# Kernel tuning notes

Hardware: AMD Instinct MI355X
Metric: run time of the kernel (lower is better)

Reference implementation:

```python
import jax, jax.numpy as jnp
import numpy as np

B, N, LATENT, HIDDEN = 65536, 32, 32, 64

def setup_inputs() -> dict:
    key = jax.random.key(0)
    ks = jax.random.split(key, 16)
    def xavier(k, shape):
        fan_in, fan_out = shape[1], shape[0]
        lim = float(np.sqrt(6.0 / (fan_in + fan_out)))
        return jax.random.uniform(k, shape, jnp.float32, -lim, lim)
    inp = {
        'x_sensors': jax.random.normal(ks[0], (B, N), jnp.float32),
        'state_x': jax.random.uniform(ks[1], (B, 1), jnp.float32),
        # GAT: W Linear(1, LATENT, bias=False), a Linear(2*LATENT, 1, bias=False), xavier init
        'W_gat': xavier(ks[2], (LATENT, 1)),
        'a_gat': xavier(ks[3], (1, 2 * LATENT)),
        # pooling: Linear(LATENT, LATENT//2) -> Tanh -> Linear(LATENT//2, 1) -> Softmax(dim=1)
        'p1_w': xavier(ks[4], (LATENT // 2, LATENT)),
        'p1_b': jnp.zeros((LATENT // 2,), jnp.float32),
        'p2_w': xavier(ks[5], (1, LATENT // 2)),
        'p2_b': jnp.zeros((1,), jnp.float32),
        # MNN: MonotonicLinear raw weights uniform(-0.5, 0.5), zero bias
        'm1_w': jax.random.uniform(ks[6], (HIDDEN, 1), jnp.float32, -0.5, 0.5),
        'm1_b': jnp.zeros((HIDDEN,), jnp.float32),
        'm2_w': jax.random.uniform(ks[7], (HIDDEN, HIDDEN), jnp.float32, -0.5, 0.5),
        'm2_b': jnp.zeros((HIDDEN,), jnp.float32),
        'm3_w': jax.random.uniform(ks[8], (LATENT, HIDDEN), jnp.float32, -0.5, 0.5),
        'm3_b': jnp.zeros((LATENT,), jnp.float32),
    }
    return inp

def reference(x_sensors, state_x, W_gat, a_gat, p1_w, p1_b, p2_w, p2_b,
              m1_w, m1_b, m2_w, m2_b, m3_w, m3_b):
    # --- GAT encoder ---
    # h = x_sensors[..., None] (B,N,1); Wh = h @ W_gat.T -> (B,N,D)
    Wh = jnp.einsum('bn,d->bnd', x_sensors, W_gat[:, 0])
    # e_ij = leakyrelu(a^T [Wh_i || Wh_j]) decomposed: a = [a1; a2]
    a1, a2 = a_gat[0, :LATENT], a_gat[0, LATENT:]
    s_i = jnp.einsum('bnd,d->bn', Wh, a1)  # contribution of Wh_i
    s_j = jnp.einsum('bnd,d->bn', Wh, a2)  # contribution of Wh_j
    e = jax.nn.leaky_relu(s_i[:, :, None] + s_j[:, None, :], 0.2)  # (B,N,N)
    alpha = jax.nn.softmax(e, axis=2)  # dropout is identity in eval
    h_prime = jnp.einsum('bij,bjd->bid', alpha, Wh)  # (B,N,D)
    # pooling: softmax over sensor dim (dim=1)
    t = jnp.tanh(h_prime @ p1_w.T + p1_b)
    beta = jax.nn.softmax(t @ p2_w.T + p2_b, axis=1)  # (B,N,1)
    z_enc = jnp.sum(h_prime * beta, axis=1)  # (B,D)
    # --- MNN decoder (exp-positive weights) ---
    h1 = jnp.tanh(state_x @ jnp.exp(m1_w).T + m1_b)
    h2 = jnp.tanh(h1 @ jnp.exp(m2_w).T + m2_b)
    z_dec = h2 @ jnp.exp(m3_w).T + m3_b  # (B,D)
    return (z_enc, z_dec)
```

## Files before the change

### kernel.cpp

```cpp
#include <hip/hip_runtime.h>
#include <hip/hip_bf16.h>

#define LOG2E     1.4426950408889634f
#define TWO_LOG2E 2.8853900817779268f

typedef __attribute__((ext_vector_type(8))) short    bf16x8;
typedef __attribute__((ext_vector_type(8))) _Float16 f16x8;
typedef __attribute__((ext_vector_type(4))) float    f32x4;
typedef __attribute__((ext_vector_type(2))) float    f32x2;

__device__ __forceinline__ float rcp_(float x){ return __builtin_amdgcn_rcpf(x); }
__device__ __forceinline__ float ex2_(float x){ return __builtin_amdgcn_exp2f(x); }

template<int K>
__device__ __forceinline__ float quadbc(float v){
  constexpr int ctrl = K * 0x55;
  return __int_as_float(__builtin_amdgcn_mov_dpp(__float_as_int(v), ctrl, 0xf, 0xf, true));
}

union FragB { bf16x8 v; uint32_t w[4]; uint4 u4; };
union FragH { f16x8  v; uint32_t w[4]; uint4 u4; };

__device__ __forceinline__ uint16_t f2bf(float x){
  union { __hip_bfloat16 h; uint16_t u; } c; c.h = __float2bfloat16(x); return c.u;
}
__device__ __forceinline__ float bf2f(uint16_t u){
  union { __hip_bfloat16 h; uint16_t u; } c; c.u = u; return __bfloat162float(c.h);
}
__device__ __forceinline__ uint32_t pkh(float a, float b){
  union { _Float16 h; uint16_t u; } ca, cb;
  ca.h = (_Float16)a; cb.h = (_Float16)b;
  return (uint32_t)ca.u | ((uint32_t)cb.u << 16);
}
__device__ __forceinline__ void split2(float a, float b, uint32_t& whi, uint32_t& wlo){
  uint16_t ah = f2bf(a), bh = f2bf(b);
  uint16_t al = f2bf(a - bf2f(ah)), bl_ = f2bf(b - bf2f(bh));
  whi = (uint32_t)ah | ((uint32_t)bh << 16);
  wlo = (uint32_t)al | ((uint32_t)bl_ << 16);
}
__device__ __forceinline__ void expsplit8(const float* __restrict__ src,
                                          FragB& hi, FragB& lo){
  float4 a = *(const float4*)src;
  float4 b = *(const float4*)(src + 4);
  float e0=__expf(a.x), e1=__expf(a.y), e2=__expf(a.z), e3=__expf(a.w);
  float e4=__expf(b.x), e5=__expf(b.y), e6=__expf(b.z), e7=__expf(b.w);
  split2(e0,e1, hi.w[0], lo.w[0]);
  split2(e2,e3, hi.w[1], lo.w[1]);
  split2(e4,e5, hi.w[2], lo.w[2]);
  split2(e6,e7, hi.w[3], lo.w[3]);
}
__device__ __forceinline__ void exph8(const float* __restrict__ src, FragH& out){
  float4 a = *(const float4*)src;
  float4 b = *(const float4*)(src + 4);
  out.w[0] = pkh(__expf(a.x), __expf(a.y));
  out.w[1] = pkh(__expf(a.z), __expf(a.w));
  out.w[2] = pkh(__expf(b.x), __expf(b.y));
  out.w[3] = pkh(__expf(b.z), __expf(b.w));
}

#define WS_FG1   0
#define WS_FG2H  2048
#define WS_FG2L  3072
#define WS_TBL   4096
#define WS_E1S   4608
#define WS_M1B   4672
#define WS_SCAL  4736

#define TBL_N     512
#define TBL_SCALE 25.6f
#define TBL_LO    -10.0f
#define TBL_CMAX  9.9f

__global__ __launch_bounds__(256) void IDSSM_pre(
    const float* __restrict__ Wg,  const float* __restrict__ ag,
    const float* __restrict__ p1w, const float* __restrict__ p1b,
    const float* __restrict__ p2w, const float* __restrict__ p2b,
    const float* __restrict__ m1w, const float* __restrict__ m1b,
    const float* __restrict__ m2w, const float* __restrict__ m3w,
    float* __restrict__ ws)
{
  const int blk = blockIdx.x;
  const int tid = threadIdx.x;
  const int l  = tid & 63;
  const int bl = l & 15, gt = l >> 4;
  if (blk < 2){
    const int s  = (blk*256 + tid) >> 6;
    const int mt = s >> 1, kt = s & 1;
    FragH h;
    exph8(m2w + (bl + 16*mt)*64 + 8*gt + 32*kt, h);
    *(uint4*)(ws + WS_FG1 + (size_t)(s*64 + l)*4) = h.u4;
  } else if (blk == 2){
    const int s2  = tid >> 6;
    const int mt2 = s2 >> 1, kt2 = s2 & 1;
    FragB hi, lo;
    expsplit8(m3w + (bl + 16*mt2)*64 + 8*gt + 32*kt2, hi, lo);
    *(uint4*)(ws + WS_FG2H + (size_t)(s2*64 + l)*4) = hi.u4;
    *(uint4*)(ws + WS_FG2L + (size_t)(s2*64 + l)*4) = lo.u4;
  } else if (blk == 3){
    __shared__ float qs[16], pb_[16], pw[16], u0s[1];
    if (tid < 16){
      float acc = 0.f;
      #pragma unroll
      for (int d = 0; d < 32; ++d) acc += p1w[tid*32 + d] * Wg[d];
      qs[tid]  = acc * TWO_LOG2E;
      pb_[tid] = p1b[tid] * TWO_LOG2E;
      pw[tid]  = -2.f * p2w[tid];
    }
    if (tid == 16){
      float sp = 0.f;
      #pragma unroll
      for (int k = 0; k < 16; ++k) sp += p2w[k];
      u0s[0] = sp + p2b[0];
    }
    __syncthreads();
    #pragma unroll
    for (int rep = 0; rep < 2; ++rep){
      const int n = tid + rep*256;
      const float c = TBL_LO + (float)n * (1.0f/TBL_SCALE);
      float u = u0s[0];
      #pragma unroll
      for (int k = 0; k < 16; ++k){
        float E = ex2_(fmaf(c, qs[k], pb_[k]));
        u = fmaf(pw[k], rcp_(E + 1.f), u);
      }
      ws[WS_TBL + n] = u * LOG2E;
    }
  } else {
    if (tid < 64){
      ws[WS_E1S + tid] = __expf(m1w[tid]) * TWO_LOG2E;
      ws[WS_M1B + tid] = m1b[tid] * TWO_LOG2E;
    } else if (tid == 64){
      float A1 = 0.f, A2 = 0.f;
      #pragma unroll
      for (int d = 0; d < 32; ++d){ A1 += Wg[d]*ag[d]; A2 += Wg[d]*ag[32+d]; }
      ws[WS_SCAL + 0] = A1 * LOG2E;
      ws[WS_SCAL + 1] = A2 * LOG2E;
    }
  }
}

#define XJ(J) (((((J)&3))==0) ? xr4[(J)>>2].x : ((((J)&3))==1) ? xr4[(J)>>2].y : \
               ((((J)&3))==2) ? xr4[(J)>>2].z : xr4[(J)>>2].w)

#define ATT_J(JQ, JR) { \
    const float Fj_ = quadbc<JQ>(Fjr[JR]); \
    const float Fq_ = quadbc<JQ>(Fqr[JR]); \
    const float xj_ = XJ(JQ*8+JR); \
    const f32x2 Fj2_ = {Fj_,Fj_}, Fq2_ = {Fq_,Fq_}, xj2_ = {xj_,xj_}; \
    f32x2 pe_; \
    pe_ = __builtin_elementwise_max(Ei2[0]*Fj2_, Eq2[0]*Fq2_); s2[0] = s2[0] + pe_; sx2[0] = sx2[0] + pe_*xj2_; \
    pe_ = __builtin_elementwise_max(Ei2[1]*Fj2_, Eq2[1]*Fq2_); s2[1] = s2[1] + pe_; sx2[1] = sx2[1] + pe_*xj2_; \
    pe_ = __builtin_elementwise_max(Ei2[2]*Fj2_, Eq2[2]*Fq2_); s2[2] = s2[2] + pe_; sx2[2] = sx2[2] + pe_*xj2_; \
    pe_ = __builtin_elementwise_max(Ei2[3]*Fj2_, Eq2[3]*Fq2_); s2[3] = s2[3] + pe_; sx2[3] = sx2[3] + pe_*xj2_; \
  }
#define ATT_Q(JQ) ATT_J(JQ,0) ATT_J(JQ,1) ATT_J(JQ,2) ATT_J(JQ,3) \
                  ATT_J(JQ,4) ATT_J(JQ,5) ATT_J(JQ,6) ATT_J(JQ,7)

__global__ __launch_bounds__(256, 4) void IDSSM_main(
    const float* __restrict__ xs,  const float* __restrict__ stx,
    const float* __restrict__ Wg,  const float* __restrict__ m2b,
    const float* __restrict__ m3b, const float* __restrict__ ws,
    float* __restrict__ out, int B)
{
  __shared__ float tbl[TBL_N];
  const int tid = threadIdx.x;
  const int lb  = tid >> 2;
  const int q   = tid & 3;
  const int b0  = blockIdx.x * 64;
  const int b   = b0 + lb;
  const bool valid = (b < B);
  const int rsrc = valid ? b : (B - 1);

  const float2 tco = *(const float2*)(ws + WS_TBL + tid*2);
  const float A1p = ws[WS_SCAL + 0];
  const float A2p = ws[WS_SCAL + 1];

  const float4* xrow4 = (const float4*)(xs + (size_t)rsrc*32);
  float4 xr4[8];
  #pragma unroll
  for (int t = 0; t < 8; ++t) xr4[t] = xrow4[t];
  float4 xia = xrow4[q*2], xib = xrow4[q*2 + 1];
  float xi[8] = { xia.x, xia.y, xia.z, xia.w, xib.x, xib.y, xib.z, xib.w };

  tbl[tid*2]     = tco.x;
  tbl[tid*2 + 1] = tco.y;

  float Fjr[8], Fqr[8];
  #pragma unroll
  for (int t = 0; t < 8; ++t){
    const float tv = A2p * xi[t];
    Fjr[t] = ex2_(tv);
    Fqr[t] = ex2_(0.2f * tv);
  }
  f32x2 Ei2[4], Eq2[4], s2[4], sx2[4];
  #pragma unroll
  for (int p = 0; p < 4; ++p){
    const float sa = A1p * xi[2*p], sb = A1p * xi[2*p + 1];
    Ei2[p] = (f32x2){ ex2_(sa), ex2_(sb) };
    Eq2[p] = (f32x2){ ex2_(0.2f*sa), ex2_(0.2f*sb) };
    s2[p]  = (f32x2)(0.f);
    sx2[p] = (f32x2)(0.f);
  }
  ATT_Q(0) ATT_Q(1) ATT_Q(2) ATT_Q(3)

  __syncthreads();

  float Zs = 0.f, Zd = 0.f;
  #pragma unroll
  for (int p = 0; p < 4; ++p){
    #pragma unroll
    for (int h = 0; h < 2; ++h){
      const float sv  = h ? s2[p].y  : s2[p].x;
      const float sxv = h ? sx2[p].y : sx2[p].x;
      const float c  = sxv * rcp_(sv);
      const float cc = fminf(fmaxf(c, TBL_LO), TBL_CMAX);
      const float f  = (cc - TBL_LO) * TBL_SCALE;
      const int   n  = (int)f;
      const float fr = f - (float)n;
      const float t0 = tbl[n];
      const float t1 = tbl[n + 1];
      const float eb = ex2_(fmaf(fr, t1 - t0, t0));
      Zs = fmaf(eb, c, Zs);
      Zd += eb;
    }
  }
  Zs += __shfl_xor(Zs, 1);  Zd += __shfl_xor(Zd, 1);
  Zs += __shfl_xor(Zs, 2);  Zd += __shfl_xor(Zd, 2);
  const float Z = Zs * rcp_(Zd);

  if (valid){
    const float4 w0 = ((const float4*)Wg)[q*2 + 0];
    const float4 w1 = ((const float4*)Wg)[q*2 + 1];
    float4* o = (float4*)(out + (size_t)b*32 + q*8);
    o[0] = make_float4(Z*w0.x, Z*w0.y, Z*w0.z, Z*w0.w);
    o[1] = make_float4(Z*w1.x, Z*w1.y, Z*w1.z, Z*w1.w);
  }

  const int lane = tid & 63;
  const int wv   = tid >> 6;
  const int gt   = lane >> 4;
  const int bl   = lane & 15;
  const int bd   = b0 + wv*16 + bl;
  const float sx0 = stx[(bd < B) ? bd : (B-1)];

  uint4 fg1r[8];
  #pragma unroll
  for (int s = 0; s < 8; ++s)
    fg1r[s] = *(const uint4*)(ws + WS_FG1 + (size_t)(s*64 + lane)*4);

  FragH h1f[2];
  #pragma unroll
  for (int kt = 0; kt < 2; ++kt){
    const int g0 = 8*gt + 32*kt;
    const float4* e1p = (const float4*)(ws + WS_E1S + g0);
    const float4* m1p = (const float4*)(ws + WS_M1B + g0);
    float4 ea = e1p[0], eb4 = e1p[1];
    float4 ma = m1p[0], mb4 = m1p[1];
    float ev[8] = { ea.x,ea.y,ea.z,ea.w, eb4.x,eb4.y,eb4.z,eb4.w };
    float mv[8] = { ma.x,ma.y,ma.z,ma.w, mb4.x,mb4.y,mb4.z,mb4.w };
    float hv[8];
    #pragma unroll
    for (int j = 0; j < 8; ++j){
      float E = ex2_(fmaf(sx0, ev[j], mv[j]));
      hv[j] = fmaf(-2.f, rcp_(E + 1.f), 1.f);
    }
    #pragma unroll
    for (int jw = 0; jw < 4; ++jw)
      h1f[kt].w[jw] = pkh(hv[2*jw], hv[2*jw+1]);
  }

  f32x4 acc[4];
  #pragma unroll
  for (int mt = 0; mt < 4; ++mt){
    float4 bi = *(const float4*)(m2b + 16*mt + 4*gt);
    acc[mt][0]=bi.x; acc[mt][1]=bi.y; acc[mt][2]=bi.z; acc[mt][3]=bi.w;
  }
  #pragma unroll
  for (int mt = 0; mt < 4; ++mt){
    #pragma unroll
    for (int kt = 0; kt < 2; ++kt){
      FragH A; A.u4 = fg1r[mt*2 + kt];
      acc[mt] = __builtin_amdgcn_mfma_f32_16x16x32_f16(A.v, h1f[kt].v, acc[mt], 0, 0, 0);
    }
  }

  uint4 fg2h[4], fg2l[4];
  #pragma unroll
  for (int s = 0; s < 4; ++s){
    fg2h[s] = *(const uint4*)(ws + WS_FG2H + (size_t)(s*64 + lane)*4);
    fg2l[s] = *(const uint4*)(ws + WS_FG2L + (size_t)(s*64 + lane)*4);
  }

  uint32_t Whi[4][2], Wlo[4][2];
  #pragma unroll
  for (int mt = 0; mt < 4; ++mt){
    float t0 = fmaf(-2.f, rcp_(ex2_(acc[mt][0]*TWO_LOG2E) + 1.f), 1.f);
    float t1 = fmaf(-2.f, rcp_(ex2_(acc[mt][1]*TWO_LOG2E) + 1.f), 1.f);
    float t2 = fmaf(-2.f, rcp_(ex2_(acc[mt][2]*TWO_LOG2E) + 1.f), 1.f);
    float t3 = fmaf(-2.f, rcp_(ex2_(acc[mt][3]*TWO_LOG2E) + 1.f), 1.f);
    split2(t0, t1, Whi[mt][0], Wlo[mt][0]);
    split2(t2, t3, Whi[mt][1], Wlo[mt][1]);
  }

  FragB B2hi[2], B2lo[2];
  const int hiSel = gt >> 1;
  #pragma unroll
  for (int kt2 = 0; kt2 < 2; ++kt2){
    #pragma unroll
    for (int jw = 0; jw < 4; ++jw){
      const int sl = bl + 16*(((jw>>1) + 2*gt) & 3);
      const int w  = jw & 1;
      uint32_t c0 = (uint32_t)__shfl((int)Whi[2*kt2+0][w], sl);
      uint32_t c1 = (uint32_t)__shfl((int)Whi[2*kt2+1][w], sl);
      B2hi[kt2].w[jw] = hiSel ? c1 : c0;
      uint32_t d0 = (uint32_t)__shfl((int)Wlo[2*kt2+0][w], sl);
      uint32_t d1 = (uint32_t)__shfl((int)Wlo[2*kt2+1][w], sl);
      B2lo[kt2].w[jw] = hiSel ? d1 : d0;
    }
  }

  f32x4 acc2[2];
  #pragma unroll
  for (int mt2 = 0; mt2 < 2; ++mt2){
    float4 bi = *(const float4*)(m3b + 16*mt2 + 4*gt);
    acc2[mt2][0]=bi.x; acc2[mt2][1]=bi.y; acc2[mt2][2]=bi.z; acc2[mt2][3]=bi.w;
  }
  #pragma unroll
  for (int mt2 = 0; mt2 < 2; ++mt2){
    #pragma unroll
    for (int kt2 = 0; kt2 < 2; ++kt2){
      FragB Ahi, Alo;
      Ahi.u4 = fg2h[mt2*2 + kt2];
      Alo.u4 = fg2l[mt2*2 + kt2];
      acc2[mt2] = __builtin_amdgcn_mfma_f32_16x16x32_bf16(Ahi.v, B2hi[kt2].v, acc2[mt2], 0, 0, 0);
      acc2[mt2] = __builtin_amdgcn_mfma_f32_16x16x32_bf16(Ahi.v, B2lo[kt2].v, acc2[mt2], 0, 0, 0);
      acc2[mt2] = __builtin_amdgcn_mfma_f32_16x16x32_bf16(Alo.v, B2hi[kt2].v, acc2[mt2], 0, 0, 0);
    }
  }

  if (bd < B){
    float* o = out + (size_t)B*32 + (size_t)bd*32;
    *(float4*)(o + 4*gt)      = make_float4(acc2[0][0], acc2[0][1], acc2[0][2], acc2[0][3]);
    *(float4*)(o + 16 + 4*gt) = make_float4(acc2[1][0], acc2[1][1], acc2[1][2], acc2[1][3]);
  }
}

extern "C" void kernel_launch(void* const* d_in, const int* in_sizes, int n_in,
                              void* d_out, int out_size, void* d_ws, size_t ws_size,
                              hipStream_t stream)
{
  const float* xs  = (const float*)d_in[0];
  const float* stx = (const float*)d_in[1];
  const float* Wg  = (const float*)d_in[2];
  const float* ag  = (const float*)d_in[3];
  const float* p1w = (const float*)d_in[4];
  const float* p1b = (const float*)d_in[5];
  const float* p2w = (const float*)d_in[6];
  const float* p2b = (const float*)d_in[7];
  const float* m1w = (const float*)d_in[8];
  const float* m1b = (const float*)d_in[9];
  const float* m2w = (const float*)d_in[10];
  const float* m2b = (const float*)d_in[11];
  const float* m3w = (const float*)d_in[12];
  const float* m3b = (const float*)d_in[13];
  float* out = (float*)d_out;
  float* ws  = (float*)d_ws;
  const int B = in_sizes[0] / 32;

  hipLaunchKernelGGL(IDSSM_pre, dim3(5), dim3(256), 0, stream,
                     Wg, ag, p1w, p1b, p2w, p2b, m1w, m1b, m2w, m3w, ws);
  const int nblk = (B + 63) / 64;
  hipLaunchKernelGGL(IDSSM_main, dim3(nblk), dim3(256), 0, stream,
                     xs, stx, Wg, m2b, m3b, ws, out, B);
}
```

Before: 25.74 us.

## Split fused kernel into separate encoder and decoder kernels with 8 lanes per row

The single fused kernel is split into two launches: an encoder kernel that maps 8 threads to each batch row (4 sensors each), and a separate decoder kernel holding the MNN MFMA path. In the encoder, each lane now loads one float4 instead of the whole row. Partner-lane sensor values and exponentials are fetched by a shuffle, and the other columns are broadcast with DPP, which lowers register pressure and allows launch bounds of 8 blocks per SM. The cost is an extra kernel launch and losing overlap between the encoder and decoder phases within one block.

```diff
diff --git a/kernel.cpp b/kernel.cpp
--- a/kernel.cpp
+++ b/kernel.cpp
@@ -139,75 +139,76 @@
   }
 }
 
-#define XJ(J) (((((J)&3))==0) ? xr4[(J)>>2].x : ((((J)&3))==1) ? xr4[(J)>>2].y : \
-               ((((J)&3))==2) ? xr4[(J)>>2].z : xr4[(J)>>2].w)
-
-#define ATT_J(JQ, JR) { \
-    const float Fj_ = quadbc<JQ>(Fjr[JR]); \
-    const float Fq_ = quadbc<JQ>(Fqr[JR]); \
-    const float xj_ = XJ(JQ*8+JR); \
+
+#define EATT_J(SX, SF, SQ, JQ, JR) { \
+    const float Fj_ = quadbc<JQ>(SF[JR]); \
+    const float Fq_ = quadbc<JQ>(SQ[JR]); \
+    const float xj_ = quadbc<JQ>(SX[JR]); \
     const f32x2 Fj2_ = {Fj_,Fj_}, Fq2_ = {Fq_,Fq_}, xj2_ = {xj_,xj_}; \
     f32x2 pe_; \
     pe_ = __builtin_elementwise_max(Ei2[0]*Fj2_, Eq2[0]*Fq2_); s2[0] = s2[0] + pe_; sx2[0] = sx2[0] + pe_*xj2_; \
     pe_ = __builtin_elementwise_max(Ei2[1]*Fj2_, Eq2[1]*Fq2_); s2[1] = s2[1] + pe_; sx2[1] = sx2[1] + pe_*xj2_; \
-    pe_ = __builtin_elementwise_max(Ei2[2]*Fj2_, Eq2[2]*Fq2_); s2[2] = s2[2] + pe_; sx2[2] = sx2[2] + pe_*xj2_; \
-    pe_ = __builtin_elementwise_max(Ei2[3]*Fj2_, Eq2[3]*Fq2_); s2[3] = s2[3] + pe_; sx2[3] = sx2[3] + pe_*xj2_; \
-  }
-#define ATT_Q(JQ) ATT_J(JQ,0) ATT_J(JQ,1) ATT_J(JQ,2) ATT_J(JQ,3) \
-                  ATT_J(JQ,4) ATT_J(JQ,5) ATT_J(JQ,6) ATT_J(JQ,7)
-
-__global__ __launch_bounds__(256, 4) void IDSSM_main(
-    const float* __restrict__ xs,  const float* __restrict__ stx,
-    const float* __restrict__ Wg,  const float* __restrict__ m2b,
-    const float* __restrict__ m3b, const float* __restrict__ ws,
-    float* __restrict__ out, int B)
+  }
+#define EATT_Q(SX, SF, SQ, JQ) \
+    EATT_J(SX,SF,SQ,JQ,0) EATT_J(SX,SF,SQ,JQ,1) EATT_J(SX,SF,SQ,JQ,2) EATT_J(SX,SF,SQ,JQ,3)
+#define EATT_ALL(SX, SF, SQ) \
+    EATT_Q(SX,SF,SQ,0) EATT_Q(SX,SF,SQ,1) EATT_Q(SX,SF,SQ,2) EATT_Q(SX,SF,SQ,3)
+
+__global__ __launch_bounds__(256, 8) void IDSSM_enc(
+    const float* __restrict__ xs, const float* __restrict__ Wg,
+    const float* __restrict__ ws, float* __restrict__ out, int B)
 {
   __shared__ float tbl[TBL_N];
   const int tid = threadIdx.x;
-  const int lb  = tid >> 2;
-  const int q   = tid & 3;
-  const int b0  = blockIdx.x * 64;
+  const int lb  = tid >> 3;
+  const int r   = tid & 7;
+  const int b0  = blockIdx.x * 32;
   const int b   = b0 + lb;
   const bool valid = (b < B);
   const int rsrc = valid ? b : (B - 1);
 
   const float2 tco = *(const float2*)(ws + WS_TBL + tid*2);
+  tbl[tid*2]     = tco.x;
+  tbl[tid*2 + 1] = tco.y;
+
   const float A1p = ws[WS_SCAL + 0];
   const float A2p = ws[WS_SCAL + 1];
 
-  const float4* xrow4 = (const float4*)(xs + (size_t)rsrc*32);
-  float4 xr4[8];
-  #pragma unroll
-  for (int t = 0; t < 8; ++t) xr4[t] = xrow4[t];
-  float4 xia = xrow4[q*2], xib = xrow4[q*2 + 1];
-  float xi[8] = { xia.x, xia.y, xia.z, xia.w, xib.x, xib.y, xib.z, xib.w };
-
-  tbl[tid*2]     = tco.x;
-  tbl[tid*2 + 1] = tco.y;
-
-  float Fjr[8], Fqr[8];
-  #pragma unroll
-  for (int t = 0; t < 8; ++t){
+  const float4 xv = *(const float4*)(xs + (size_t)rsrc*32 + r*4);
+  float xi[4] = { xv.x, xv.y, xv.z, xv.w };
+
+  float Fjr[4], Fqr[4];
+  #pragma unroll
+  for (int t = 0; t < 4; ++t){
     const float tv = A2p * xi[t];
     Fjr[t] = ex2_(tv);
     Fqr[t] = ex2_(0.2f * tv);
   }
-  f32x2 Ei2[4], Eq2[4], s2[4], sx2[4];
-  #pragma unroll
-  for (int p = 0; p < 4; ++p){
+  float xo[4], Fo[4], Fqo[4];
+  #pragma unroll
+  for (int t = 0; t < 4; ++t){
+    xo[t]  = __shfl_xor(xi[t], 4);
+    Fo[t]  = __shfl_xor(Fjr[t], 4);
+    Fqo[t] = __shfl_xor(Fqr[t], 4);
+  }
+
+  f32x2 Ei2[2], Eq2[2], s2[2], sx2[2];
+  #pragma unroll
+  for (int p = 0; p < 2; ++p){
     const float sa = A1p * xi[2*p], sb = A1p * xi[2*p + 1];
     Ei2[p] = (f32x2){ ex2_(sa), ex2_(sb) };
     Eq2[p] = (f32x2){ ex2_(0.2f*sa), ex2_(0.2f*sb) };
     s2[p]  = (f32x2)(0.f);
     sx2[p] = (f32x2)(0.f);
   }
-  ATT_Q(0) ATT_Q(1) ATT_Q(2) ATT_Q(3)
+  EATT_ALL(xi, Fjr, Fqr)
+  EATT_ALL(xo, Fo,  Fqo)
 
   __syncthreads();
 
   float Zs = 0.f, Zd = 0.f;
   #pragma unroll
-  for (int p = 0; p < 4; ++p){
+  for (int p = 0; p < 2; ++p){
     #pragma unroll
     for (int h = 0; h < 2; ++h){
       const float sv  = h ? s2[p].y  : s2[p].x;
@@ -226,16 +227,23 @@
   }
   Zs += __shfl_xor(Zs, 1);  Zd += __shfl_xor(Zd, 1);
   Zs += __shfl_xor(Zs, 2);  Zd += __shfl_xor(Zd, 2);
+  Zs += __shfl_xor(Zs, 4);  Zd += __shfl_xor(Zd, 4);
   const float Z = Zs * rcp_(Zd);
 
   if (valid){
-    const float4 w0 = ((const float4*)Wg)[q*2 + 0];
-    const float4 w1 = ((const float4*)Wg)[q*2 + 1];
-    float4* o = (float4*)(out + (size_t)b*32 + q*8);
-    o[0] = make_float4(Z*w0.x, Z*w0.y, Z*w0.z, Z*w0.w);
-    o[1] = make_float4(Z*w1.x, Z*w1.y, Z*w1.z, Z*w1.w);
-  }
-
+    const float4 w = ((const float4*)Wg)[r];
+    *(float4*)(out + (size_t)b*32 + r*4) =
+        make_float4(Z*w.x, Z*w.y, Z*w.z, Z*w.w);
+  }
+}
+
+__global__ __launch_bounds__(256, 4) void IDSSM_dec(
+    const float* __restrict__ stx, const float* __restrict__ m2b,
+    const float* __restrict__ m3b, const float* __restrict__ ws,
+    float* __restrict__ out, int B)
+{
+  const int tid = threadIdx.x;
+  const int b0  = blockIdx.x * 64;
   const int lane = tid & 63;
   const int wv   = tid >> 6;
   const int gt   = lane >> 4;
@@ -369,7 +377,10 @@
 
   hipLaunchKernelGGL(IDSSM_pre, dim3(5), dim3(256), 0, stream,
                      Wg, ag, p1w, p1b, p2w, p2b, m1w, m1b, m2w, m3w, ws);
-  const int nblk = (B + 63) / 64;
-  hipLaunchKernelGGL(IDSSM_main, dim3(nblk), dim3(256), 0, stream,
-                     xs, stx, Wg, m2b, m3b, ws, out, B);
-}
+  const int nbe = (B + 31) / 32;
+  hipLaunchKernelGGL(IDSSM_enc, dim3(nbe), dim3(256), 0, stream,
+                     xs, Wg, ws, out, B);
+  const int nbd = (B + 63) / 64;
+  hipLaunchKernelGGL(IDSSM_dec, dim3(nbd), dim3(256), 0, stream,
+                     stx, m2b, m3b, ws, out, B);
+}
```

New measurement: 28.50 us. 1.11x slower.
